# Performance work log

Measured on AMD Instinct MI355X. Metric: run time of the kernel, lower is better.

The kernel has to match this reference:

```python
import jax, jax.numpy as jnp
import numpy as np

N_HIT = 30000   # hits per plane
N_EDGE = 90000  # Delaunay planar edges per plane (~3N)
N_SP = 30000    # spacepoints
H = 128         # hidden dim
F_IN = 4        # wire, time, integral, rms
N_CLASS = 5     # semantic classes
N_ITERS = 3     # core message-passing iterations
PLANES = ("u", "v", "y")


def setup_inputs() -> dict:
    key = jax.random.key(0)
    ks = iter(jax.random.split(key, 64))
    inp = {}
    for p in PLANES:
        inp[f"x_{p}"] = jax.random.normal(next(ks), (N_HIT, F_IN), jnp.float32)
        inp[f"edge_{p}"] = jax.random.randint(next(ks), (2, N_EDGE), 0, N_HIT)
        # row 0: hit index in plane, row 1: spacepoint index
        inp[f"nexus_{p}"] = jax.random.randint(next(ks), (2, N_SP), 0, N_HIT)
    def lin(k, i, o):
        return (jax.random.normal(k, (i, o), jnp.float32) / np.sqrt(i)).astype(jnp.float32)
    inp["W_enc"] = lin(next(ks), F_IN, H); inp["b_enc"] = jnp.zeros((H,), jnp.float32)
    inp["W_msg1"] = lin(next(ks), 2 * H, H); inp["b_msg1"] = jnp.zeros((H,), jnp.float32)
    inp["W_msg2"] = lin(next(ks), H, H); inp["b_msg2"] = jnp.zeros((H,), jnp.float32)
    inp["W_upd"] = lin(next(ks), 2 * H, H); inp["b_upd"] = jnp.zeros((H,), jnp.float32)
    inp["W_sp"] = lin(next(ks), H, H); inp["b_sp"] = jnp.zeros((H,), jnp.float32)
    inp["W_nx"] = lin(next(ks), 2 * H, H); inp["b_nx"] = jnp.zeros((H,), jnp.float32)
    inp["W_sem"] = lin(next(ks), H, N_CLASS); inp["b_sem"] = jnp.zeros((N_CLASS,), jnp.float32)
    return inp


def _segment_mean(data, ids, num):
    s = jax.ops.segment_sum(data, ids, num_segments=num)
    c = jax.ops.segment_sum(jnp.ones((ids.shape[0],), data.dtype), ids, num_segments=num)
    return s / jnp.maximum(c, 1.0)[:, None]


def _core(hs, edges, nexus, W_msg1, b_msg1, W_msg2, b_msg2, W_upd, b_upd,
          W_sp, b_sp, W_nx, b_nx):
    # --- planar convolution per plane (gather-transform-scatter) ---
    new_hs = []
    for h, e in zip(hs, edges):
        src, dst = e[0], e[1]
        m = jnp.concatenate([h[dst], h[src]], axis=-1)          # [E, 2H]
        m = jax.nn.relu(m @ W_msg1 + b_msg1) @ W_msg2 + b_msg2  # [E, H]
        agg = _segment_mean(m, dst, h.shape[0])                 # [N, H]
        upd = jax.nn.relu(jnp.concatenate([h, agg], -1) @ W_upd + b_upd)
        new_hs.append(h + upd)
    hs = new_hs
    # --- nexus convolution: planes -> spacepoints -> planes ---
    sp = jnp.zeros((N_SP, hs[0].shape[1]), hs[0].dtype)
    for h, nx in zip(hs, nexus):
        sp = sp + _segment_mean(h[nx[0]], nx[1], N_SP)
    sp = jax.nn.relu(sp @ W_sp + b_sp)                          # [N_SP, H]
    out_hs = []
    for h, nx in zip(hs, nexus):
        back = _segment_mean(sp[nx[1]], nx[0], h.shape[0])      # [N, H]
        upd = jax.nn.relu(jnp.concatenate([h, back], -1) @ W_nx + b_nx)
        out_hs.append(h + upd)
    return out_hs


def reference(x_u, x_v, x_y, edge_u, edge_v, edge_y, nexus_u, nexus_v, nexus_y,
              W_enc, b_enc, W_msg1, b_msg1, W_msg2, b_msg2, W_upd, b_upd,
              W_sp, b_sp, W_nx, b_nx, W_sem, b_sem):
    edges = (edge_u, edge_v, edge_y)
    nexus = (nexus_u, nexus_v, nexus_y)
    # encoder
    hs = [jax.nn.relu(x @ W_enc + b_enc) for x in (x_u, x_v, x_y)]
    # core message-passing iterations (planar + nexus)
    for _ in range(N_ITERS):
        hs = _core(hs, edges, nexus, W_msg1, b_msg1, W_msg2, b_msg2,
                   W_upd, b_upd, W_sp, b_sp, W_nx, b_nx)
    # semantic decoder per plane
    return tuple(h @ W_sem + b_sem for h in hs)
```

## Files before the change

### kernel.cpp

```cpp
#include <hip/hip_runtime.h>
#include <hip/hip_fp16.h>

#define N_HITS 30000
#define N_EDGES 90000
#define N_SPS 30000
#define HD 128
#define NCLS 5

#define PADM 136

typedef __attribute__((ext_vector_type(8))) __bf16 bf16x8;
typedef __attribute__((ext_vector_type(4))) float floatx4;

__device__ __forceinline__ float2 b2f2(uint u) {
    union { uint u; __bf16 b[2]; } x; x.u = u;
    return make_float2((float)x.b[0], (float)x.b[1]);
}
__device__ __forceinline__ uint f2b2(float a, float b) {
    union { uint u; __bf16 b[2]; } x; x.b[0] = (__bf16)a; x.b[1] = (__bf16)b;
    return x.u;
}

__global__ void enc_kernel(const float* __restrict__ xu, const float* __restrict__ xv,
                           const float* __restrict__ xy, const float* __restrict__ W,
                           const float* __restrict__ b, __bf16* __restrict__ h) {
    int gid = blockIdx.x * blockDim.x + threadIdx.x;
    if (gid >= 3 * N_HITS * HD) return;
    int j = gid & (HD - 1);
    int n = (gid >> 7) % N_HITS;
    int p = gid / (N_HITS * HD);
    const float* x = (p == 0) ? xu : (p == 1) ? xv : xy;
    float acc = b[j];
#pragma unroll
    for (int k = 0; k < 4; ++k) acc = fmaf(x[n * 4 + k], W[k * HD + j], acc);
    h[gid] = (__bf16)fmaxf(acc, 0.f);
}

__global__ void hist_all_kernel(const int* __restrict__ eu, const int* __restrict__ ev,
                                const int* __restrict__ ey, const int* __restrict__ nu,
                                const int* __restrict__ nv, const int* __restrict__ ny,
                                int* __restrict__ cnt) {
    int gid = blockIdx.x * blockDim.x + threadIdx.x;
    if (gid >= 450000) return;
    int p = gid / 150000;
    int r = gid - p * 150000;
    const int* e = (p == 0) ? eu : (p == 1) ? ev : ey;
    const int* nx = (p == 0) ? nu : (p == 1) ? nv : ny;
    if (r < N_EDGES) {
        atomicAdd(&cnt[p * 30000 + e[N_EDGES + r]], 1);
    } else if (r < N_EDGES + N_SPS) {
        int i = r - N_EDGES;
        atomicAdd(&cnt[(3 + p) * 30000 + nx[N_SPS + i]], 1);
    } else {
        int i = r - N_EDGES - N_SPS;
        atomicAdd(&cnt[(6 + p) * 30000 + nx[i]], 1);
    }
}

__launch_bounds__(1024)
__global__ void scan_kernel(const int* __restrict__ cnt, int* __restrict__ off,
                            int* __restrict__ cursor) {
    int seg = blockIdx.x;
    const int* c = cnt + seg * 30000;
    int* o = off + seg * 30001;
    int* cur = cursor + seg * 30000;
    int t = threadIdx.x;
    int base = t * 30;
    int lc[30];
    int sum = 0;
#pragma unroll
    for (int k = 0; k < 30; ++k) {
        int i = base + k;
        lc[k] = (i < 30000) ? c[i] : 0;
        sum += lc[k];
    }
    __shared__ int part[1024];
    part[t] = sum;
    __syncthreads();
    for (int d = 1; d < 1024; d <<= 1) {
        int x = (t >= d) ? part[t - d] : 0;
        __syncthreads();
        part[t] += x;
        __syncthreads();
    }
    int run = part[t] - sum;
#pragma unroll
    for (int k = 0; k < 30; ++k) {
        int i = base + k;
        if (i < 30000) { o[i] = run; cur[i] = run; run += lc[k]; }
    }
    if (t == 1023) o[30000] = part[1023];
}

__global__ void fill_kernel(const int* __restrict__ eu, const int* __restrict__ ev,
                            const int* __restrict__ ey, const int* __restrict__ nu,
                            const int* __restrict__ nv, const int* __restrict__ ny,
                            int* __restrict__ cursor, int* __restrict__ csr_e,
                            int* __restrict__ csr_s, int* __restrict__ csr_h) {
    int gid = blockIdx.x * blockDim.x + threadIdx.x;
    if (gid >= 450000) return;
    int p = gid / 150000;
    int r = gid - p * 150000;
    const int* e = (p == 0) ? eu : (p == 1) ? ev : ey;
    const int* nx = (p == 0) ? nu : (p == 1) ? nv : ny;
    if (r < N_EDGES) {
        int d = e[N_EDGES + r];
        int pos = atomicAdd(&cursor[p * 30000 + d], 1);
        csr_e[p * N_EDGES + pos] = e[r];
    } else if (r < N_EDGES + N_SPS) {
        int i = r - N_EDGES;
        int spid = nx[N_SPS + i];
        int pos = atomicAdd(&cursor[(3 + p) * 30000 + spid], 1);
        csr_s[p * N_SPS + pos] = nx[i];
    } else {
        int i = r - N_EDGES - N_SPS;
        int hit = nx[i];
        int pos = atomicAdd(&cursor[(6 + p) * 30000 + hit], 1);
        csr_h[p * N_SPS + pos] = nx[N_SPS + i];
    }
}

__device__ __forceinline__ void pack4(const float* __restrict__ W, __bf16* __restrict__ P,
                                      int idx, int koff) {
    int j = idx & 7, lane = (idx >> 3) & 63, ks = (idx >> 9) & 3, n = (idx >> 11) & 7;
    int k = ks * 32 + (lane >> 4) * 8 + j, col = n * 16 + (lane & 15);
    P[idx] = (__bf16)W[(k + koff) * 128 + col];
}
__device__ __forceinline__ void pack8(const float* __restrict__ W, __bf16* __restrict__ P, int idx) {
    int j = idx & 7, lane = (idx >> 3) & 63, ks = (idx >> 9) & 7, n = (idx >> 12) & 7;
    int k = ks * 32 + (lane >> 4) * 8 + j, col = n * 16 + (lane & 15);
    P[idx] = (__bf16)W[k * 128 + col];
}

__global__ void wprep_kernel(const float* __restrict__ W1, const float* __restrict__ W2,
                             const float* __restrict__ Wu, const float* __restrict__ Wn,
                             const float* __restrict__ Wsp, __bf16* __restrict__ packs) {
    int gid = blockIdx.x * blockDim.x + threadIdx.x;
    if (gid < 16384) { pack4(W1, packs, gid, 0); return; }
    gid -= 16384;
    if (gid < 16384) { pack4(W1, packs + 16384, gid, 128); return; }
    gid -= 16384;
    if (gid < 16384) { pack4(W2, packs + 32768, gid, 0); return; }
    gid -= 16384;
    if (gid < 32768) { pack8(Wu, packs + 49152, gid); return; }
    gid -= 32768;
    if (gid < 32768) { pack8(Wn, packs + 81920, gid); return; }
    gid -= 32768;
    if (gid < 16384) { pack4(Wsp, packs + 114688, gid, 0); }
}

__launch_bounds__(256, 4)
__global__ void y_init_kernel(const __bf16* __restrict__ h, const __bf16* __restrict__ W1sP,
                              __bf16* __restrict__ y_s) {
    __shared__ __bf16 sA[128 * PADM];
    int t = threadIdx.x;
    int n0b = blockIdx.x * 128;
    const int M = 3 * N_HITS;
    for (int i = t; i < 2048; i += 256) {
        int row = i >> 4, c = i & 15;
        int n = n0b + row; if (n >= M) n = M - 1;
        *(uint4*)&sA[row * PADM + c * 8] = ((const uint4*)(h + (size_t)n * HD))[c];
    }
    __syncthreads();

    int lane = t & 63, wave = t >> 6;
    int lcol = lane & 15, quad = lane >> 4;
    int nt0 = wave * 2;
    bool odd = (lcol & 1) != 0;

    const bf16x8* wp = (const bf16x8*)W1sP;
    bf16x8 B[2][4];
#pragma unroll
    for (int nt = 0; nt < 2; ++nt)
#pragma unroll
        for (int ks = 0; ks < 4; ++ks)
            B[nt][ks] = wp[((nt0 + nt) * 4 + ks) * 64 + lane];
    floatx4 acc[8][2];
#pragma unroll
    for (int mt = 0; mt < 8; ++mt) { acc[mt][0] = (floatx4){0,0,0,0}; acc[mt][1] = (floatx4){0,0,0,0}; }
#pragma unroll
    for (int mt = 0; mt < 8; ++mt)
#pragma unroll
        for (int ks = 0; ks < 4; ++ks) {
            bf16x8 a = *(const bf16x8*)&sA[(mt * 16 + lcol) * PADM + ks * 32 + quad * 8];
            acc[mt][0] = __builtin_amdgcn_mfma_f32_16x16x32_bf16(a, B[0][ks], acc[mt][0], 0, 0, 0);
            acc[mt][1] = __builtin_amdgcn_mfma_f32_16x16x32_bf16(a, B[1][ks], acc[mt][1], 0, 0, 0);
        }
    __syncthreads();
#pragma unroll
    for (int mt = 0; mt < 8; ++mt)
#pragma unroll
        for (int r = 0; r < 4; ++r) {
            float v0 = acc[mt][0][r], v1 = acc[mt][1][r];
            float p0 = __shfl_xor(v0, 1), p1 = __shfl_xor(v1, 1);
            float av = odd ? p1 : v0, bv = odd ? v1 : p0;
            int col = nt0 * 16 + (odd ? 15 + lcol : lcol);
            *(uint*)&sA[(mt * 16 + quad * 4 + r) * PADM + col] = f2b2(av, bv);
        }
    __syncthreads();
    for (int i = t; i < 2048; i += 256) {
        int row = i >> 4, c = i & 15;
        int n = n0b + row;
        if (n < M) ((uint4*)(y_s + (size_t)n * HD))[c] = *(uint4*)&sA[row * PADM + c * 8];
    }
}

__launch_bounds__(256, 4)
__global__ void update_planar_kernel(__bf16* __restrict__ h, const __bf16* __restrict__ y_s,
                                     const int* __restrict__ off, const int* __restrict__ csr_e,
                                     const float* __restrict__ b1, const __bf16* __restrict__ W1dP,
                                     const __bf16* __restrict__ W2P, const float* __restrict__ b2,
                                     const __bf16* __restrict__ WuP, const float* __restrict__ bu) {
    int p = blockIdx.y;
    __bf16* hp = h + (size_t)p * N_HITS * HD;
    const __bf16* ysp = y_s + (size_t)p * N_HITS * HD;
    const int* o = off + p * 30001;
    const int* csr = csr_e + p * N_EDGES;

    __shared__ __bf16 sH[64 * PADM];
    __shared__ __bf16 sA[64 * PADM];
    int t = threadIdx.x;
    int n0b = blockIdx.x * 64;
    int lane = t & 63, wave = t >> 6;
    int lcol = lane & 15, quad = lane >> 4;
    int nt0 = wave * 2;
    bool odd = (lcol & 1) != 0;

    for (int i = t; i < 1024; i += 256) {
        int row = i >> 4, c = i & 15;
        int n = n0b + row; if (n >= N_HITS) n = N_HITS - 1;
        *(uint4*)&sH[row * PADM + c * 8] = ((const uint4*)(hp + (size_t)n * HD))[c];
    }
    __syncthreads();
    floatx4 yd[4][2], accU[4][2];
    {
        const bf16x8* w1 = (const bf16x8*)W1dP;
        const bf16x8* wu = (const bf16x8*)WuP;
        bf16x8 B1[2][4], BU[2][4];
#pragma unroll
        for (int nt = 0; nt < 2; ++nt)
#pragma unroll
            for (int ks = 0; ks < 4; ++ks) {
                B1[nt][ks] = w1[((nt0 + nt) * 4 + ks) * 64 + lane];
                BU[nt][ks] = wu[((nt0 + nt) * 8 + ks) * 64 + lane];
            }
#pragma unroll
        for (int nt = 0; nt < 2; ++nt) {
            float bv = bu[(nt0 + nt) * 16 + lcol];
#pragma unroll
            for (int mt = 0; mt < 4; ++mt) {
                yd[mt][nt] = (floatx4){0, 0, 0, 0};
                accU[mt][nt] = (floatx4){bv, bv, bv, bv};
            }
        }
#pragma unroll
        for (int mt = 0; mt < 4; ++mt)
#pragma unroll
            for (int ks = 0; ks < 4; ++ks) {
                bf16x8 a = *(const bf16x8*)&sH[(mt * 16 + lcol) * PADM + ks * 32 + quad * 8];
                yd[mt][0] = __builtin_amdgcn_mfma_f32_16x16x32_bf16(a, B1[0][ks], yd[mt][0], 0, 0, 0);
                yd[mt][1] = __builtin_amdgcn_mfma_f32_16x16x32_bf16(a, B1[1][ks], yd[mt][1], 0, 0, 0);
                accU[mt][0] = __builtin_amdgcn_mfma_f32_16x16x32_bf16(a, BU[0][ks], accU[mt][0], 0, 0, 0);
                accU[mt][1] = __builtin_amdgcn_mfma_f32_16x16x32_bf16(a, BU[1][ks], accU[mt][1], 0, 0, 0);
            }
    }
#pragma unroll
    for (int mt = 0; mt < 4; ++mt)
#pragma unroll
        for (int r = 0; r < 4; ++r) {
            float v0 = yd[mt][0][r], v1 = yd[mt][1][r];
            float p0 = __shfl_xor(v0, 1), p1 = __shfl_xor(v1, 1);
            float av = odd ? p1 : v0, bv = odd ? v1 : p0;
            int col = nt0 * 16 + (odd ? 15 + lcol : lcol);
            *(uint*)&sA[(mt * 16 + quad * 4 + r) * PADM + col] = f2b2(av, bv);
        }
    __syncthreads();
    for (int i = t; i < 1024; i += 256) {
        int row = i >> 4, c = i & 15;
        int d = n0b + row; if (d >= N_HITS) d = N_HITS - 1;
        int beg = o[d], end = o[d + 1];
        union { uint4 u; __bf16 b[8]; } ydv;
        ydv.u = *(uint4*)&sA[row * PADM + c * 8];
        float4 b1a = *(const float4*)(b1 + c * 8);
        float4 b1b = *(const float4*)(b1 + c * 8 + 4);
        float bb[8] = {b1a.x, b1a.y, b1a.z, b1a.w, b1b.x, b1b.y, b1b.z, b1b.w};
        float a8[8] = {0, 0, 0, 0, 0, 0, 0, 0};
        for (int k = beg; k < end; ++k) {
            int s = csr[k];
            union { uint4 u; __bf16 b[8]; } ys;
            ys.u = ((const uint4*)(ysp + (size_t)s * HD))[c];
#pragma unroll
            for (int j = 0; j < 8; ++j)
                a8[j] += fmaxf((float)ydv.b[j] + (float)ys.b[j] + bb[j], 0.f);
        }
        float iv = (end > beg) ? 1.f / (float)(end - beg) : 0.f;
        union { __bf16 o8[8]; uint4 u; } outv;
#pragma unroll
        for (int j = 0; j < 8; ++j) outv.o8[j] = (__bf16)(a8[j] * iv);
        *(uint4*)&sA[row * PADM + c * 8] = outv.u;
    }
    __syncthreads();
    floatx4 agg[4][2];
    {
        const bf16x8* w2p = (const bf16x8*)W2P;
        bf16x8 B[2][4];
#pragma unroll
        for (int nt = 0; nt < 2; ++nt)
#pragma unroll
            for (int ks = 0; ks < 4; ++ks)
                B[nt][ks] = w2p[((nt0 + nt) * 4 + ks) * 64 + lane];
#pragma unroll
        for (int nt = 0; nt < 2; ++nt) {
            float bv = b2[(nt0 + nt) * 16 + lcol];
#pragma unroll
            for (int mt = 0; mt < 4; ++mt) agg[mt][nt] = (floatx4){bv, bv, bv, bv};
        }
#pragma unroll
        for (int mt = 0; mt < 4; ++mt)
#pragma unroll
            for (int ks = 0; ks < 4; ++ks) {
                bf16x8 a = *(const bf16x8*)&sA[(mt * 16 + lcol) * PADM + ks * 32 + quad * 8];
                agg[mt][0] = __builtin_amdgcn_mfma_f32_16x16x32_bf16(a, B[0][ks], agg[mt][0], 0, 0, 0);
                agg[mt][1] = __builtin_amdgcn_mfma_f32_16x16x32_bf16(a, B[1][ks], agg[mt][1], 0, 0, 0);
            }
    }
    __syncthreads();
#pragma unroll
    for (int mt = 0; mt < 4; ++mt)
#pragma unroll
        for (int r = 0; r < 4; ++r) {
            float v0 = agg[mt][0][r], v1 = agg[mt][1][r];
            float p0 = __shfl_xor(v0, 1), p1 = __shfl_xor(v1, 1);
            float av = odd ? p1 : v0, bv = odd ? v1 : p0;
            int col = nt0 * 16 + (odd ? 15 + lcol : lcol);
            *(uint*)&sA[(mt * 16 + quad * 4 + r) * PADM + col] = f2b2(av, bv);
        }
    __syncthreads();
    {
        const bf16x8* wu = (const bf16x8*)WuP;
        bf16x8 B[2][4];
#pragma unroll
        for (int nt = 0; nt < 2; ++nt)
#pragma unroll
            for (int ks = 0; ks < 4; ++ks)
                B[nt][ks] = wu[((nt0 + nt) * 8 + 4 + ks) * 64 + lane];
#pragma unroll
        for (int mt = 0; mt < 4; ++mt)
#pragma unroll
            for (int ks = 0; ks < 4; ++ks) {
                bf16x8 a = *(const bf16x8*)&sA[(mt * 16 + lcol) * PADM + ks * 32 + quad * 8];
                accU[mt][0] = __builtin_amdgcn_mfma_f32_16x16x32_bf16(a, B[0][ks], accU[mt][0], 0, 0, 0);
                accU[mt][1] = __builtin_amdgcn_mfma_f32_16x16x32_bf16(a, B[1][ks], accU[mt][1], 0, 0, 0);
            }
    }
    __syncthreads();
#pragma unroll
    for (int mt = 0; mt < 4; ++mt)
#pragma unroll
        for (int r = 0; r < 4; ++r) {
            float v0 = fmaxf(accU[mt][0][r], 0.f), v1 = fmaxf(accU[mt][1][r], 0.f);
            float p0 = __shfl_xor(v0, 1), p1 = __shfl_xor(v1, 1);
            float av = odd ? p1 : v0, bv = odd ? v1 : p0;
            int col = nt0 * 16 + (odd ? 15 + lcol : lcol);
            uint* sp2 = (uint*)&sH[(mt * 16 + quad * 4 + r) * PADM + col];
            float2 ho = b2f2(*sp2);
            *sp2 = f2b2(ho.x + av, ho.y + bv);
        }
    __syncthreads();
    for (int i = t; i < 1024; i += 256) {
        int row = i >> 4, c = i & 15;
        int n = n0b + row;
        if (n < N_HITS) ((uint4*)(hp + (size_t)n * HD))[c] = *(uint4*)&sH[row * PADM + c * 8];
    }
}

__launch_bounds__(256, 4)
__global__ void sp_fused_kernel(const __bf16* __restrict__ h, const int* __restrict__ off,
                                const int* __restrict__ csr_s, const __bf16* __restrict__ WspP,
                                const float* __restrict__ b, __bf16* __restrict__ spf) {
    __shared__ __bf16 sA[64 * PADM];
    int t = threadIdx.x;
    int n0b = blockIdx.x * 64;
    int lane = t & 63, wave = t >> 6;
    int lcol = lane & 15, quad = lane >> 4;
    int nt0 = wave * 2;
    bool odd = (lcol & 1) != 0;

    for (int i = t; i < 1024; i += 256) {
        int row = i >> 4, c = i & 15;
        int s = n0b + row; if (s >= N_SPS) s = N_SPS - 1;
        float a8[8] = {0, 0, 0, 0, 0, 0, 0, 0};
#pragma unroll
        for (int p = 0; p < 3; ++p) {
            const int* o = off + (3 + p) * 30001;
            int beg = o[s], end = o[s + 1];
            const int* csr = csr_s + p * N_SPS;
            const __bf16* hb = h + (size_t)p * N_HITS * HD;
            float s8[8] = {0, 0, 0, 0, 0, 0, 0, 0};
            for (int k = beg; k < end; ++k) {
                int hit = csr[k];
                union { uint4 u; __bf16 b[8]; } hv;
                hv.u = ((const uint4*)(hb + (size_t)hit * HD))[c];
#pragma unroll
                for (int j = 0; j < 8; ++j) s8[j] += (float)hv.b[j];
            }
            float iv = (end > beg) ? 1.f / (float)(end - beg) : 0.f;
#pragma unroll
            for (int j = 0; j < 8; ++j) a8[j] += s8[j] * iv;
        }
        union { __bf16 o8[8]; uint4 u; } outv;
#pragma unroll
        for (int j = 0; j < 8; ++j) outv.o8[j] = (__bf16)a8[j];
        *(uint4*)&sA[row * PADM + c * 8] = outv.u;
    }
    __syncthreads();

    const bf16x8* wp = (const bf16x8*)WspP;
    bf16x8 B[2][4];
#pragma unroll
    for (int nt = 0; nt < 2; ++nt)
#pragma unroll
        for (int ks = 0; ks < 4; ++ks)
            B[nt][ks] = wp[((nt0 + nt) * 4 + ks) * 64 + lane];

    floatx4 acc[4][2];
#pragma unroll
    for (int nt = 0; nt < 2; ++nt) {
        float bv = b[(nt0 + nt) * 16 + lcol];
#pragma unroll
        for (int mt = 0; mt < 4; ++mt) acc[mt][nt] = (floatx4){bv, bv, bv, bv};
    }
#pragma unroll
    for (int mt = 0; mt < 4; ++mt)
#pragma unroll
        for (int ks = 0; ks < 4; ++ks) {
            bf16x8 a = *(const bf16x8*)&sA[(mt * 16 + lcol) * PADM + ks * 32 + quad * 8];
            acc[mt][0] = __builtin_amdgcn_mfma_f32_16x16x32_bf16(a, B[0][ks], acc[mt][0], 0, 0, 0);
            acc[mt][1] = __builtin_amdgcn_mfma_f32_16x16x32_bf16(a, B[1][ks], acc[mt][1], 0, 0, 0);
        }
    __syncthreads();
#pragma unroll
    for (int mt = 0; mt < 4; ++mt)
#pragma unroll
        for (int r = 0; r < 4; ++r) {
            float v0 = fmaxf(acc[mt][0][r], 0.f), v1 = fmaxf(acc[mt][1][r], 0.f);
            float p0 = __shfl_xor(v0, 1), p1 = __shfl_xor(v1, 1);
            float av = odd ? p1 : v0, bv = odd ? v1 : p0;
            int col = nt0 * 16 + (odd ? 15 + lcol : lcol);
            *(uint*)&sA[(mt * 16 + quad * 4 + r) * PADM + col] = f2b2(av, bv);
        }
    __syncthreads();
    for (int i = t; i < 1024; i += 256) {
        int row = i >> 4, c = i & 15;
        int n = n0b + row;
        if (n < N_SPS) ((uint4*)(spf + (size_t)n * HD))[c] = *(uint4*)&sA[row * PADM + c * 8];
    }
}

__launch_bounds__(256, 4)
__global__ void update_y_kernel(__bf16* __restrict__ h, const __bf16* __restrict__ sp,
                                const int* __restrict__ off, const int* __restrict__ csr_h,
                                const __bf16* __restrict__ WP, const float* __restrict__ b,
                                const __bf16* __restrict__ W1sP, __bf16* __restrict__ y_s) {
    int p = blockIdx.y;
    __bf16* hp = h + (size_t)p * N_HITS * HD;
    __bf16* ysp = y_s + (size_t)p * N_HITS * HD;
    const int* o = off + (6 + p) * 30001;
    const int* csr = csr_h + p * N_SPS;

    __shared__ __bf16 sH[64 * PADM];
    __shared__ __bf16 sA[64 * PADM];
    int t = threadIdx.x;
    int n0b = blockIdx.x * 64;
    int lane = t & 63, wave = t >> 6;
    int lcol = lane & 15, quad = lane >> 4;
    int nt0 = wave * 2;
    bool odd = (lcol & 1) != 0;

    for (int i = t; i < 1024; i += 256) {
        int row = i >> 4, c = i & 15;
        int hit = n0b + row; if (hit >= N_HITS) hit = N_HITS - 1;
        int beg = o[hit], end = o[hit + 1];
        float a8[8] = {0, 0, 0, 0, 0, 0, 0, 0};
        for (int k = beg; k < end; ++k) {
            int spid = csr[k];
            union { uint4 u; __bf16 b[8]; } sv;
            sv.u = ((const uint4*)(sp + (size_t)spid * HD))[c];
#pragma unroll
            for (int j = 0; j < 8; ++j) a8[j] += (float)sv.b[j];
        }
        float iv = (end > beg) ? 1.f / (float)(end - beg) : 0.f;
        union { __bf16 o8[8]; uint4 u; } outv;
#pragma unroll
        for (int j = 0; j < 8; ++j) outv.o8[j] = (__bf16)(a8[j] * iv);
        *(uint4*)&sA[row * PADM + c * 8] = outv.u;
    }
    for (int i = t; i < 1024; i += 256) {
        int row = i >> 4, c = i & 15;
        int n = n0b + row; if (n >= N_HITS) n = N_HITS - 1;
        *(uint4*)&sH[row * PADM + c * 8] = ((const uint4*)(hp + (size_t)n * HD))[c];
    }
    __syncthreads();
    floatx4 acc[4][2];
    {
        const bf16x8* wp = (const bf16x8*)WP;
        bf16x8 BH[2][4], BA[2][4];
#pragma unroll
        for (int nt = 0; nt < 2; ++nt)
#pragma unroll
            for (int ks = 0; ks < 4; ++ks) {
                BH[nt][ks] = wp[((nt0 + nt) * 8 + ks) * 64 + lane];
                BA[nt][ks] = wp[((nt0 + nt) * 8 + 4 + ks) * 64 + lane];
            }
#pragma unroll
        for (int nt = 0; nt < 2; ++nt) {
            float bv = b[(nt0 + nt) * 16 + lcol];
#pragma unroll
            for (int mt = 0; mt < 4; ++mt) acc[mt][nt] = (floatx4){bv, bv, bv, bv};
        }
#pragma unroll
        for (int mt = 0; mt < 4; ++mt)
#pragma unroll
            for (int ks = 0; ks < 4; ++ks) {
                bf16x8 ah = *(const bf16x8*)&sH[(mt * 16 + lcol) * PADM + ks * 32 + quad * 8];
                bf16x8 aa = *(const bf16x8*)&sA[(mt * 16 + lcol) * PADM + ks * 32 + quad * 8];
                acc[mt][0] = __builtin_amdgcn_mfma_f32_16x16x32_bf16(ah, BH[0][ks], acc[mt][0], 0, 0, 0);
                acc[mt][1] = __builtin_amdgcn_mfma_f32_16x16x32_bf16(ah, BH[1][ks], acc[mt][1], 0, 0, 0);
                acc[mt][0] = __builtin_amdgcn_mfma_f32_16x16x32_bf16(aa, BA[0][ks], acc[mt][0], 0, 0, 0);
                acc[mt][1] = __builtin_amdgcn_mfma_f32_16x16x32_bf16(aa, BA[1][ks], acc[mt][1], 0, 0, 0);
            }
    }
    __syncthreads();
#pragma unroll
    for (int mt = 0; mt < 4; ++mt)
#pragma unroll
        for (int r = 0; r < 4; ++r) {
            float v0 = fmaxf(acc[mt][0][r], 0.f), v1 = fmaxf(acc[mt][1][r], 0.f);
            float p0 = __shfl_xor(v0, 1), p1 = __shfl_xor(v1, 1);
            float av = odd ? p1 : v0, bv = odd ? v1 : p0;
            int col = nt0 * 16 + (odd ? 15 + lcol : lcol);
            uint* sp2 = (uint*)&sH[(mt * 16 + quad * 4 + r) * PADM + col];
            float2 ho = b2f2(*sp2);
            *sp2 = f2b2(ho.x + av, ho.y + bv);
        }
    __syncthreads();
    for (int i = t; i < 1024; i += 256) {
        int row = i >> 4, c = i & 15;
        int n = n0b + row;
        if (n < N_HITS) ((uint4*)(hp + (size_t)n * HD))[c] = *(uint4*)&sH[row * PADM + c * 8];
    }
    {
        const bf16x8* wyp = (const bf16x8*)W1sP;
        bf16x8 B[2][4];
#pragma unroll
        for (int nt = 0; nt < 2; ++nt)
#pragma unroll
            for (int ks = 0; ks < 4; ++ks)
                B[nt][ks] = wyp[((nt0 + nt) * 4 + ks) * 64 + lane];
        floatx4 yacc[4][2];
#pragma unroll
        for (int mt = 0; mt < 4; ++mt) { yacc[mt][0] = (floatx4){0,0,0,0}; yacc[mt][1] = (floatx4){0,0,0,0}; }
#pragma unroll
        for (int mt = 0; mt < 4; ++mt)
#pragma unroll
            for (int ks = 0; ks < 4; ++ks) {
                bf16x8 a = *(const bf16x8*)&sH[(mt * 16 + lcol) * PADM + ks * 32 + quad * 8];
                yacc[mt][0] = __builtin_amdgcn_mfma_f32_16x16x32_bf16(a, B[0][ks], yacc[mt][0], 0, 0, 0);
                yacc[mt][1] = __builtin_amdgcn_mfma_f32_16x16x32_bf16(a, B[1][ks], yacc[mt][1], 0, 0, 0);
            }
#pragma unroll
        for (int mt = 0; mt < 4; ++mt)
#pragma unroll
            for (int r = 0; r < 4; ++r) {
                float v0 = yacc[mt][0][r], v1 = yacc[mt][1][r];
                float p0 = __shfl_xor(v0, 1), p1 = __shfl_xor(v1, 1);
                float av = odd ? p1 : v0, bv = odd ? v1 : p0;
                int col = nt0 * 16 + (odd ? 15 + lcol : lcol);
                *(uint*)&sA[(mt * 16 + quad * 4 + r) * PADM + col] = f2b2(av, bv);
            }
    }
    __syncthreads();
    for (int i = t; i < 1024; i += 256) {
        int row = i >> 4, c = i & 15;
        int n = n0b + row;
        if (n < N_HITS) ((uint4*)(ysp + (size_t)n * HD))[c] = *(uint4*)&sA[row * PADM + c * 8];
    }
}

__global__ void dec_kernel(const __bf16* __restrict__ h, const float* __restrict__ W,
                           const float* __restrict__ b, float* __restrict__ out) {
    __shared__ float sW[640];
    __shared__ float sB[8];
    int t = threadIdx.x;
    for (int i = t; i < 640; i += 256) sW[i] = W[i];
    if (t < 5) sB[t] = b[t];
    __syncthreads();
    int n = blockIdx.x * 256 + t;
    if (n >= 3 * N_HITS) return;
    const uint4* hr = (const uint4*)(h + (size_t)n * HD);
    float a0 = sB[0], a1 = sB[1], a2 = sB[2], a3 = sB[3], a4 = sB[4];
#pragma unroll 4
    for (int q = 0; q < 16; ++q) {
        union { uint4 u; __bf16 bb[8]; } v; v.u = hr[q];
        const float* w = &sW[q * 40];
#pragma unroll
        for (int j = 0; j < 8; ++j) {
            float x = (float)v.bb[j];
            a0 = fmaf(x, w[j * 5 + 0], a0);
            a1 = fmaf(x, w[j * 5 + 1], a1);
            a2 = fmaf(x, w[j * 5 + 2], a2);
            a3 = fmaf(x, w[j * 5 + 3], a3);
            a4 = fmaf(x, w[j * 5 + 4], a4);
        }
    }
    float* oo = out + (size_t)n * NCLS;
    oo[0] = a0; oo[1] = a1; oo[2] = a2; oo[3] = a3; oo[4] = a4;
}

extern "C" void kernel_launch(void* const* d_in, const int* in_sizes, int n_in,
                              void* d_out, int out_size, void* d_ws, size_t ws_size,
                              hipStream_t stream) {
    const float* xu = (const float*)d_in[0];
    const int* eu = (const int*)d_in[1];
    const int* nu = (const int*)d_in[2];
    const float* xv = (const float*)d_in[3];
    const int* ev = (const int*)d_in[4];
    const int* nv = (const int*)d_in[5];
    const float* xy = (const float*)d_in[6];
    const int* ey = (const int*)d_in[7];
    const int* ny = (const int*)d_in[8];
    const float* W_enc = (const float*)d_in[9];
    const float* b_enc = (const float*)d_in[10];
    const float* W1 = (const float*)d_in[11];
    const float* b1 = (const float*)d_in[12];
    const float* W2 = (const float*)d_in[13];
    const float* b2 = (const float*)d_in[14];
    const float* W_upd = (const float*)d_in[15];
    const float* b_upd = (const float*)d_in[16];
    const float* W_sp = (const float*)d_in[17];
    const float* b_sp = (const float*)d_in[18];
    const float* W_nx = (const float*)d_in[19];
    const float* b_nx = (const float*)d_in[20];
    const float* W_sem = (const float*)d_in[21];
    const float* b_sem = (const float*)d_in[22];

    const size_t HN = (size_t)3 * N_HITS * HD;
    __bf16* h = (__bf16*)d_ws;
    __bf16* y_s = h + HN;
    __bf16* sp = y_s + HN;
    int* cnt = (int*)(sp + (size_t)N_SPS * HD);
    int* off = cnt + 270000;
    int* cursor = off + 270009;
    int* csr_e = cursor + 270000;
    int* csr_s = csr_e + 270000;
    int* csr_h = csr_s + 90000;
    __bf16* packs = (__bf16*)(csr_h + 90000);
    __bf16* W1dP = packs;
    __bf16* W1sP = packs + 16384;
    __bf16* W2P = packs + 32768;
    __bf16* WuP = packs + 49152;
    __bf16* WnP = packs + 81920;
    __bf16* WspP = packs + 114688;

    wprep_kernel<<<512, 256, 0, stream>>>(W1, W2, W_upd, W_nx, W_sp, packs);
    (void)hipMemsetAsync(cnt, 0, 270000 * sizeof(int), stream);
    hist_all_kernel<<<(450000 + 255) / 256, 256, 0, stream>>>(eu, ev, ey, nu, nv, ny, cnt);
    scan_kernel<<<9, 1024, 0, stream>>>(cnt, off, cursor);
    fill_kernel<<<(450000 + 255) / 256, 256, 0, stream>>>(eu, ev, ey, nu, nv, ny,
                                                          cursor, csr_e, csr_s, csr_h);

    enc_kernel<<<(3 * N_HITS * HD + 255) / 256, 256, 0, stream>>>(xu, xv, xy, W_enc, b_enc, h);
    y_init_kernel<<<(3 * N_HITS + 127) / 128, 256, 0, stream>>>(h, W1sP, y_s);

    for (int it = 0; it < 3; ++it) {
        update_planar_kernel<<<dim3((N_HITS + 63) / 64, 3), 256, 0, stream>>>(
            h, y_s, off, csr_e, b1, W1dP, W2P, b2, WuP, b_upd);
        sp_fused_kernel<<<(N_SPS + 63) / 64, 256, 0, stream>>>(h, off, csr_s, WspP, b_sp, sp);
        update_y_kernel<<<dim3((N_HITS + 63) / 64, 3), 256, 0, stream>>>(
            h, sp, off, csr_h, WnP, b_nx, W1sP, y_s);
    }

    dec_kernel<<<(3 * N_HITS + 255) / 256, 256, 0, stream>>>(h, W_sem, b_sem, (float*)d_out);
}
```

Baseline: 599.8 us.

## Fuse encoder into y-init kernel and stage CSR offsets/indices in LDS

Merges the encoder into the y_init kernel, so the hidden state is computed in registers, written to shared memory and global memory once, and no longer re-read. In the planar, spacepoint and nexus-back gather kernels, the per-block CSR offsets and neighbour indices are preloaded cooperatively into shared memory, with a global fallback when a block's edge count exceeds a fixed cap. This removes per-thread redundant global offset/index loads from the gather loops. The cost is extra LDS use and barriers, which may lower occupancy.

```diff
diff --git a/kernel.cpp b/kernel.cpp
--- a/kernel.cpp
+++ b/kernel.cpp
@@ -19,21 +19,6 @@
 __device__ __forceinline__ uint f2b2(float a, float b) {
     union { uint u; __bf16 b[2]; } x; x.b[0] = (__bf16)a; x.b[1] = (__bf16)b;
     return x.u;
-}
-
-__global__ void enc_kernel(const float* __restrict__ xu, const float* __restrict__ xv,
-                           const float* __restrict__ xy, const float* __restrict__ W,
-                           const float* __restrict__ b, __bf16* __restrict__ h) {
-    int gid = blockIdx.x * blockDim.x + threadIdx.x;
-    if (gid >= 3 * N_HITS * HD) return;
-    int j = gid & (HD - 1);
-    int n = (gid >> 7) % N_HITS;
-    int p = gid / (N_HITS * HD);
-    const float* x = (p == 0) ? xu : (p == 1) ? xv : xy;
-    float acc = b[j];
-#pragma unroll
-    for (int k = 0; k < 4; ++k) acc = fmaf(x[n * 4 + k], W[k * HD + j], acc);
-    h[gid] = (__bf16)fmaxf(acc, 0.f);
 }
 
 __global__ void hist_all_kernel(const int* __restrict__ eu, const int* __restrict__ ev,
@@ -150,8 +135,10 @@
 }
 
 __launch_bounds__(256, 4)
-__global__ void y_init_kernel(const __bf16* __restrict__ h, const __bf16* __restrict__ W1sP,
-                              __bf16* __restrict__ y_s) {
+__global__ void enc_y_kernel(const float* __restrict__ xu, const float* __restrict__ xv,
+                             const float* __restrict__ xy, const float* __restrict__ We,
+                             const float* __restrict__ be, const __bf16* __restrict__ W1sP,
+                             __bf16* __restrict__ h, __bf16* __restrict__ y_s) {
     __shared__ __bf16 sA[128 * PADM];
     int t = threadIdx.x;
     int n0b = blockIdx.x * 128;
@@ -159,7 +146,23 @@
     for (int i = t; i < 2048; i += 256) {
         int row = i >> 4, c = i & 15;
         int n = n0b + row; if (n >= M) n = M - 1;
-        *(uint4*)&sA[row * PADM + c * 8] = ((const uint4*)(h + (size_t)n * HD))[c];
+        int p = n / N_HITS;
+        int nn = n - p * N_HITS;
+        const float* x = (p == 0) ? xu : (p == 1) ? xv : xy;
+        float4 xv4 = *(const float4*)(x + nn * 4);
+        union { __bf16 o8[8]; uint4 u; } outv;
+#pragma unroll
+        for (int j = 0; j < 8; ++j) {
+            int col = c * 8 + j;
+            float acc = be[col];
+            acc = fmaf(xv4.x, We[0 * HD + col], acc);
+            acc = fmaf(xv4.y, We[1 * HD + col], acc);
+            acc = fmaf(xv4.z, We[2 * HD + col], acc);
+            acc = fmaf(xv4.w, We[3 * HD + col], acc);
+            outv.o8[j] = (__bf16)fmaxf(acc, 0.f);
+        }
+        *(uint4*)&sA[row * PADM + c * 8] = outv.u;
+        if (n0b + row < M) ((uint4*)(h + (size_t)n * HD))[c] = outv.u;
     }
     __syncthreads();
 
@@ -205,6 +208,7 @@
     }
 }
 
+#define ECAP 640
 __launch_bounds__(256, 4)
 __global__ void update_planar_kernel(__bf16* __restrict__ h, const __bf16* __restrict__ y_s,
                                      const int* __restrict__ off, const int* __restrict__ csr_e,
@@ -219,6 +223,8 @@
 
     __shared__ __bf16 sH[64 * PADM];
     __shared__ __bf16 sA[64 * PADM];
+    __shared__ int sOff[65];
+    __shared__ int sIdx[ECAP];
     int t = threadIdx.x;
     int n0b = blockIdx.x * 64;
     int lane = t & 63, wave = t >> 6;
@@ -226,12 +232,21 @@
     int nt0 = wave * 2;
     bool odd = (lcol & 1) != 0;
 
+    if (t < 65) {
+        int idx = n0b + t; if (idx > N_HITS) idx = N_HITS;
+        sOff[t] = o[idx];
+    }
     for (int i = t; i < 1024; i += 256) {
         int row = i >> 4, c = i & 15;
         int n = n0b + row; if (n >= N_HITS) n = N_HITS - 1;
         *(uint4*)&sH[row * PADM + c * 8] = ((const uint4*)(hp + (size_t)n * HD))[c];
     }
     __syncthreads();
+    int base = sOff[0];
+    int total = sOff[64] - base;
+    bool useL = (total <= ECAP);
+    if (useL) for (int i = t; i < total; i += 256) sIdx[i] = csr[base + i];
+
     floatx4 yd[4][2], accU[4][2];
     {
         const bf16x8* w1 = (const bf16x8*)W1dP;
@@ -277,8 +292,9 @@
     __syncthreads();
     for (int i = t; i < 1024; i += 256) {
         int row = i >> 4, c = i & 15;
-        int d = n0b + row; if (d >= N_HITS) d = N_HITS - 1;
-        int beg = o[d], end = o[d + 1];
+        int d = n0b + row;
+        int beg = 0, end = 0;
+        if (d < N_HITS) { beg = sOff[row]; end = sOff[row + 1]; }
         union { uint4 u; __bf16 b[8]; } ydv;
         ydv.u = *(uint4*)&sA[row * PADM + c * 8];
         float4 b1a = *(const float4*)(b1 + c * 8);
@@ -286,7 +302,7 @@
         float bb[8] = {b1a.x, b1a.y, b1a.z, b1a.w, b1b.x, b1b.y, b1b.z, b1b.w};
         float a8[8] = {0, 0, 0, 0, 0, 0, 0, 0};
         for (int k = beg; k < end; ++k) {
-            int s = csr[k];
+            int s = useL ? sIdx[k - base] : csr[k];
             union { uint4 u; __bf16 b[8]; } ys;
             ys.u = ((const uint4*)(ysp + (size_t)s * HD))[c];
 #pragma unroll
@@ -374,11 +390,14 @@
     }
 }
 
+#define SCAP 576
 __launch_bounds__(256, 4)
 __global__ void sp_fused_kernel(const __bf16* __restrict__ h, const int* __restrict__ off,
                                 const int* __restrict__ csr_s, const __bf16* __restrict__ WspP,
                                 const float* __restrict__ b, __bf16* __restrict__ spf) {
     __shared__ __bf16 sA[64 * PADM];
+    __shared__ int sOff[3][65];
+    __shared__ int sIdx[SCAP];
     int t = threadIdx.x;
     int n0b = blockIdx.x * 64;
     int lane = t & 63, wave = t >> 6;
@@ -386,27 +405,48 @@
     int nt0 = wave * 2;
     bool odd = (lcol & 1) != 0;
 
-    for (int i = t; i < 1024; i += 256) {
-        int row = i >> 4, c = i & 15;
-        int s = n0b + row; if (s >= N_SPS) s = N_SPS - 1;
+    if (t < 195) {
+        int p = t / 65, i = t - p * 65;
+        int idx = n0b + i; if (idx > N_SPS) idx = N_SPS;
+        sOff[p][i] = off[(3 + p) * 30001 + idx];
+    }
+    __syncthreads();
+    int base0 = sOff[0][0], len0 = sOff[0][64] - base0;
+    int base1 = sOff[1][0], len1 = sOff[1][64] - base1;
+    int base2 = sOff[2][0], len2 = sOff[2][64] - base2;
+    int ofs1 = len0, ofs2 = len0 + len1;
+    bool useL = (ofs2 + len2 <= SCAP);
+    if (useL) {
+        for (int i = t; i < len0; i += 256) sIdx[i] = csr_s[base0 + i];
+        for (int i = t; i < len1; i += 256) sIdx[ofs1 + i] = csr_s[N_SPS + base1 + i];
+        for (int i = t; i < len2; i += 256) sIdx[ofs2 + i] = csr_s[2 * N_SPS + base2 + i];
+    }
+    __syncthreads();
+
+    for (int i = t; i < 1024; i += 256) {
+        int row = i >> 4, c = i & 15;
+        int s = n0b + row;
         float a8[8] = {0, 0, 0, 0, 0, 0, 0, 0};
-#pragma unroll
-        for (int p = 0; p < 3; ++p) {
-            const int* o = off + (3 + p) * 30001;
-            int beg = o[s], end = o[s + 1];
-            const int* csr = csr_s + p * N_SPS;
-            const __bf16* hb = h + (size_t)p * N_HITS * HD;
-            float s8[8] = {0, 0, 0, 0, 0, 0, 0, 0};
-            for (int k = beg; k < end; ++k) {
-                int hit = csr[k];
-                union { uint4 u; __bf16 b[8]; } hv;
-                hv.u = ((const uint4*)(hb + (size_t)hit * HD))[c];
-#pragma unroll
-                for (int j = 0; j < 8; ++j) s8[j] += (float)hv.b[j];
-            }
-            float iv = (end > beg) ? 1.f / (float)(end - beg) : 0.f;
-#pragma unroll
-            for (int j = 0; j < 8; ++j) a8[j] += s8[j] * iv;
+        if (s < N_SPS) {
+#pragma unroll
+            for (int p = 0; p < 3; ++p) {
+                int beg = sOff[p][row], end = sOff[p][row + 1];
+                int bb = (p == 0) ? base0 : (p == 1) ? base1 : base2;
+                int oo = (p == 0) ? 0 : (p == 1) ? ofs1 : ofs2;
+                const int* csr = csr_s + p * N_SPS;
+                const __bf16* hb = h + (size_t)p * N_HITS * HD;
+                float s8[8] = {0, 0, 0, 0, 0, 0, 0, 0};
+                for (int k = beg; k < end; ++k) {
+                    int hit = useL ? sIdx[oo + (k - bb)] : csr[k];
+                    union { uint4 u; __bf16 b[8]; } hv;
+                    hv.u = ((const uint4*)(hb + (size_t)hit * HD))[c];
+#pragma unroll
+                    for (int j = 0; j < 8; ++j) s8[j] += (float)hv.b[j];
+                }
+                float iv = (end > beg) ? 1.f / (float)(end - beg) : 0.f;
+#pragma unroll
+                for (int j = 0; j < 8; ++j) a8[j] += s8[j] * iv;
+            }
         }
         union { __bf16 o8[8]; uint4 u; } outv;
 #pragma unroll
@@ -457,6 +497,7 @@
     }
 }
 
+#define HCAP 320
 __launch_bounds__(256, 4)
 __global__ void update_y_kernel(__bf16* __restrict__ h, const __bf16* __restrict__ sp,
                                 const int* __restrict__ off, const int* __restrict__ csr_h,
@@ -470,6 +511,8 @@
 
     __shared__ __bf16 sH[64 * PADM];
     __shared__ __bf16 sA[64 * PADM];
+    __shared__ int sOff[65];
+    __shared__ int sIdx[HCAP];
     int t = threadIdx.x;
     int n0b = blockIdx.x * 64;
     int lane = t & 63, wave = t >> 6;
@@ -477,13 +520,30 @@
     int nt0 = wave * 2;
     bool odd = (lcol & 1) != 0;
 
-    for (int i = t; i < 1024; i += 256) {
-        int row = i >> 4, c = i & 15;
-        int hit = n0b + row; if (hit >= N_HITS) hit = N_HITS - 1;
-        int beg = o[hit], end = o[hit + 1];
+    if (t < 65) {
+        int idx = n0b + t; if (idx > N_HITS) idx = N_HITS;
+        sOff[t] = o[idx];
+    }
+    for (int i = t; i < 1024; i += 256) {
+        int row = i >> 4, c = i & 15;
+        int n = n0b + row; if (n >= N_HITS) n = N_HITS - 1;
+        *(uint4*)&sH[row * PADM + c * 8] = ((const uint4*)(hp + (size_t)n * HD))[c];
+    }
+    __syncthreads();
+    int base = sOff[0];
+    int total = sOff[64] - base;
+    bool useL = (total <= HCAP);
+    if (useL) for (int i = t; i < total; i += 256) sIdx[i] = csr[base + i];
+    __syncthreads();
+
+    for (int i = t; i < 1024; i += 256) {
+        int row = i >> 4, c = i & 15;
+        int hit = n0b + row;
+        int beg = 0, end = 0;
+        if (hit < N_HITS) { beg = sOff[row]; end = sOff[row + 1]; }
         float a8[8] = {0, 0, 0, 0, 0, 0, 0, 0};
         for (int k = beg; k < end; ++k) {
-            int spid = csr[k];
+            int spid = useL ? sIdx[k - base] : csr[k];
             union { uint4 u; __bf16 b[8]; } sv;
             sv.u = ((const uint4*)(sp + (size_t)spid * HD))[c];
 #pragma unroll
@@ -494,11 +554,6 @@
 #pragma unroll
         for (int j = 0; j < 8; ++j) outv.o8[j] = (__bf16)(a8[j] * iv);
         *(uint4*)&sA[row * PADM + c * 8] = outv.u;
-    }
-    for (int i = t; i < 1024; i += 256) {
-        int row = i >> 4, c = i & 15;
-        int n = n0b + row; if (n >= N_HITS) n = N_HITS - 1;
-        *(uint4*)&sH[row * PADM + c * 8] = ((const uint4*)(hp + (size_t)n * HD))[c];
     }
     __syncthreads();
     floatx4 acc[4][2];
@@ -669,8 +724,8 @@
     fill_kernel<<<(450000 + 255) / 256, 256, 0, stream>>>(eu, ev, ey, nu, nv, ny,
                                                           cursor, csr_e, csr_s, csr_h);
 
-    enc_kernel<<<(3 * N_HITS * HD + 255) / 256, 256, 0, stream>>>(xu, xv, xy, W_enc, b_enc, h);
-    y_init_kernel<<<(3 * N_HITS + 127) / 128, 256, 0, stream>>>(h, W1sP, y_s);
+    enc_y_kernel<<<(3 * N_HITS + 127) / 128, 256, 0, stream>>>(xu, xv, xy, W_enc, b_enc,
+                                                               W1sP, h, y_s);
 
     for (int it = 0; it < 3; ++it) {
         update_planar_kernel<<<dim3((N_HITS + 63) / 64, 3), 256, 0, stream>>>(
```

New measurement: 518.2 us. 1.16x faster.
